# Optimization experiments

Hardware: AMD Instinct MI355X
Metric: run time of the kernel (lower is better)

## Reference

```python
import jax, jax.numpy as jnp
import numpy as np

DIM = 1024
NUM_HEADS = 16
HEAD_DIM = DIM // NUM_HEADS
ROPE_BASE = 10000.0


def _rope_tables(seq_len, head_dim, dtype):
    # inv_freq over even indices, then freqs duplicated (cat(freqs, freqs))
    inv_freq = 1.0 / (ROPE_BASE ** (jnp.arange(0, head_dim, 2, dtype=jnp.float32) / head_dim))
    t = jnp.arange(seq_len, dtype=jnp.float32)
    freqs = jnp.einsum('i,j->ij', t, inv_freq)          # [N, head_dim/2]
    emb = jnp.concatenate([freqs, freqs], axis=-1)      # [N, head_dim]
    return jnp.cos(emb).astype(dtype), jnp.sin(emb).astype(dtype)


def _rotate_half(x):
    x1, x2 = jnp.split(x, 2, axis=-1)
    return jnp.concatenate([-x2, x1], axis=-1)


def setup_inputs() -> dict:
    key = jax.random.key(0)
    k1, k2, k3 = jax.random.split(key, 3)
    B, N = 2, 2048
    x = jax.random.normal(k1, (B, N, DIM), dtype=jnp.float32)
    w_qkv = jax.random.normal(k2, (3 * DIM, DIM), dtype=jnp.float32) * (DIM ** -0.5)
    w_out = jax.random.normal(k3, (DIM, DIM), dtype=jnp.float32) * (DIM ** -0.5)
    return {"x": x, "w_qkv": w_qkv, "w_out": w_out}


def reference(x, w_qkv, w_out):
    B, N, C = x.shape
    scale = HEAD_DIM ** -0.5
    qkv = x @ w_qkv.T                                   # [B, N, 3*C]
    qkv = qkv.reshape(B, N, 3, NUM_HEADS, HEAD_DIM)
    qkv = jnp.transpose(qkv, (2, 0, 3, 1, 4))           # [3, B, H, N, hd]
    q, k, v = qkv[0], qkv[1], qkv[2]

    cos, sin = _rope_tables(N, HEAD_DIM, x.dtype)       # [N, hd] each
    q = q * cos + _rotate_half(q) * sin
    k = k * cos + _rotate_half(k) * sin

    attn = jnp.einsum('bhqd,bhkd->bhqk', q, k) * scale  # [B, H, N, N]
    attn = jax.nn.softmax(attn, axis=-1)
    out = jnp.einsum('bhqk,bhkd->bhqd', attn, v)        # [B, H, N, hd]
    out = jnp.transpose(out, (0, 2, 1, 3)).reshape(B, N, C)
    return out @ w_out.T
```

## Files before the change

### kernel.cpp

```cpp
#include <hip/hip_runtime.h>
#include <stdint.h>


#define BATCH 2
#define SEQ   2048
#define DIM_C 1024
#define NHEAD 16
#define HD    64
#define MTOT  (BATCH * SEQ)
#define NQKV  (3 * DIM_C)
#define QSCALE 0.1803368801111204f

typedef _Float16 h8 __attribute__((ext_vector_type(8)));
typedef _Float16 h4v __attribute__((ext_vector_type(4)));
typedef float    f4 __attribute__((ext_vector_type(4)));
typedef unsigned int u4v __attribute__((ext_vector_type(4)));

#if __has_builtin(__builtin_amdgcn_exp2f)
#define EXP2(x) __builtin_amdgcn_exp2f(x)
#else
#define EXP2(x) exp2f(x)
#endif

__device__ __forceinline__ f4 mfma16(h8 a, h8 b, f4 c) {
  return __builtin_amdgcn_mfma_f32_16x16x32_f16(a, b, c, 0, 0, 0);
}

__device__ __forceinline__ unsigned pk2(float a, float b) {
  auto t = __builtin_amdgcn_cvt_pkrtz(a, b);
  unsigned u;
  __builtin_memcpy(&u, &t, 4);
  return u;
}

__device__ __forceinline__ void swap32(unsigned& a, unsigned& b) {
#if __has_builtin(__builtin_amdgcn_permlane32_swap)
  typedef unsigned u2_ __attribute__((ext_vector_type(2)));
  u2_ r = __builtin_amdgcn_permlane32_swap(a, b, false, false);
  a = r[0]; b = r[1];
#else
  const bool hi = (threadIdx.x & 32) != 0;
  unsigned sa = __shfl_xor(a, 32), sb = __shfl_xor(b, 32);
  unsigned na = hi ? sb : a, nb = hi ? b : sa;
  a = na; b = nb;
#endif
}
__device__ __forceinline__ void swap16(unsigned& a, unsigned& b) {
#if __has_builtin(__builtin_amdgcn_permlane16_swap)
  typedef unsigned u2_ __attribute__((ext_vector_type(2)));
  u2_ r = __builtin_amdgcn_permlane16_swap(a, b, false, false);
  a = r[0]; b = r[1];
#else
  const bool hi = (threadIdx.x & 16) != 0;
  unsigned sa = __shfl_xor(a, 16), sb = __shfl_xor(b, 16);
  unsigned na = hi ? sb : a, nb = hi ? b : sa;
  a = na; b = nb;
#endif
}

__device__ __forceinline__ void gload16(const _Float16* g, _Float16* l) {
  __builtin_amdgcn_global_load_lds(
      (const __attribute__((address_space(1))) void*)g,
      (__attribute__((address_space(3))) void*)l, 16, 0, 0);
}

#define N4X  1048576
#define N4WQ 786432
#define N4WO 262144
#define CVT_TOT (N4X + N4WQ + N4WO)
__global__ void prep_kernel(const float* __restrict__ x,
                            const float* __restrict__ wq,
                            const float* __restrict__ wo,
                            _Float16* __restrict__ xh,
                            _Float16* __restrict__ wqh,
                            _Float16* __restrict__ woh,
                            float* __restrict__ cosT, float* __restrict__ sinT) {
  int idx = blockIdx.x * blockDim.x + threadIdx.x;
  if (idx < CVT_TOT) {
    const float* s; _Float16* d; int i;
    if (idx < N4X) { s = x; d = xh; i = idx; }
    else if (idx < N4X + N4WQ) { s = wq; d = wqh; i = idx - N4X; }
    else { s = wo; d = woh; i = idx - (N4X + N4WQ); }
    float4 v = reinterpret_cast<const float4*>(s)[i];
    h4v o = {(_Float16)v.x, (_Float16)v.y, (_Float16)v.z, (_Float16)v.w};
    reinterpret_cast<h4v*>(d)[i] = o;
  } else {
    int t = idx - CVT_TOT;
    int n = t >> 5, j = t & 31;
    float inv = powf(10000.0f, -(float)(2 * j) / 64.0f);
    float a = (float)n * inv;
    cosT[t] = cosf(a);
    sinT[t] = sinf(a);
  }
}

__global__ __launch_bounds__(256) void gemm_qkv(const _Float16* __restrict__ A,
                                                const _Float16* __restrict__ Bm,
                                                const float* __restrict__ cosT,
                                                const float* __restrict__ sinT,
                                                _Float16* __restrict__ qh,
                                                _Float16* __restrict__ kh,
                                                _Float16* __restrict__ vh) {
  const int K = DIM_C;
  __shared__ _Float16 Ah[2][128 * 32];
  __shared__ _Float16 Bh[2][128 * 32];
  const int tid = threadIdx.x;
  const int wave = tid >> 6, lane = tid & 63;
  const int lr = lane & 15, lg = lane >> 4;
  const int p = blockIdx.x;
  const int wg = (p & 7) * 96 + (p >> 3);
  const int bx = wg >> 5, by = wg & 31;
  const int m0 = by * 128, n0 = bx * 128;
  const int wr = (wave >> 1) * 64, wc = (wave & 1) * 64;

  const f4 zf = {0.f, 0.f, 0.f, 0.f};
  f4 acc[4][4];
#pragma unroll
  for (int i = 0; i < 4; ++i)
#pragma unroll
    for (int j = 0; j < 4; ++j) acc[i][j] = zf;

  const _Float16* Ab = A + (size_t)m0 * K;
  const _Float16* Bb = Bm + (size_t)n0 * K;

  auto stage = [&](int ks, int bi) {
#pragma unroll
    for (int it = 0; it < 2; ++it) {
      int c = tid + it * 256;
      int row = c >> 2, part = c & 3;
      gload16(Ab + (size_t)row * K + ks * 32 + part * 8, &Ah[bi][c * 8]);
      gload16(Bb + (size_t)row * K + ks * 32 + part * 8, &Bh[bi][c * 8]);
    }
  };

  stage(0, 0);
  const int ksteps = K >> 5;
  for (int ks = 0; ks < ksteps; ++ks) {
    __syncthreads();
    int cur = ks & 1;
    if (ks + 1 < ksteps) stage(ks + 1, cur ^ 1);

    h8 af[4], bf[4];
#pragma unroll
    for (int i = 0; i < 4; ++i) af[i] = *(const h8*)&Ah[cur][(wr + i * 16 + lr) * 32 + lg * 8];
#pragma unroll
    for (int j = 0; j < 4; ++j) bf[j] = *(const h8*)&Bh[cur][(wc + j * 16 + lr) * 32 + lg * 8];
#pragma unroll
    for (int i = 0; i < 4; ++i)
#pragma unroll
      for (int j = 0; j < 4; ++j) acc[i][j] = mfma16(af[i], bf[j], acc[i][j]);
  }

  const int nc = n0 + wc;
  const int s = nc >> 10;
  const int hcol = (nc >> 6) & 15;
  _Float16* dst = (s == 0) ? qh : (s == 1) ? kh : vh;
  const float scl = (s == 0) ? QSCALE : 1.0f;
#pragma unroll
  for (int i = 0; i < 4; ++i)
#pragma unroll
    for (int r = 0; r < 4; ++r) {
      int row = m0 + wr + i * 16 + lg * 4 + r;
      int n = row & (SEQ - 1);
      _Float16* drow = dst + ((size_t)(((row >> 11) * NHEAD + hcol) * SEQ + n)) * HD;
      if (s == 2) {
        drow[lr]      = (_Float16)acc[i][0][r];
        drow[lr + 16] = (_Float16)acc[i][1][r];
        drow[lr + 32] = (_Float16)acc[i][2][r];
        drow[lr + 48] = (_Float16)acc[i][3][r];
      } else {
        float c0 = cosT[n * 32 + lr],      sn0 = sinT[n * 32 + lr];
        float c1 = cosT[n * 32 + 16 + lr], sn1 = sinT[n * 32 + 16 + lr];
        float a10 = acc[i][0][r], a20 = acc[i][2][r];
        float a11 = acc[i][1][r], a21 = acc[i][3][r];
        drow[lr]      = (_Float16)((a10 * c0 - a20 * sn0) * scl);
        drow[lr + 32] = (_Float16)((a20 * c0 + a10 * sn0) * scl);
        drow[lr + 16] = (_Float16)((a11 * c1 - a21 * sn1) * scl);
        drow[lr + 48] = (_Float16)((a21 * c1 + a11 * sn1) * scl);
      }
    }
}

__global__ __launch_bounds__(256) void gemm_out(const _Float16* __restrict__ A,
                                                const _Float16* __restrict__ Bm,
                                                float* __restrict__ Cv) {
  const int K = DIM_C, N = DIM_C;
  __shared__ _Float16 Ah[2][128 * 32];
  __shared__ _Float16 Bh[2][64 * 32];
  const int tid = threadIdx.x;
  const int wave = tid >> 6, lane = tid & 63;
  const int lr = lane & 15, lg = lane >> 4;
  const int p = blockIdx.x;
  const int wg = (p & 7) * 64 + (p >> 3);
  const int bx = wg >> 5, by = wg & 31;
  const int m0 = by * 128, n0 = bx * 64;
  const int wr = (wave >> 1) * 64, wc = (wave & 1) * 32;

  const f4 zf = {0.f, 0.f, 0.f, 0.f};
  f4 acc[4][2];
#pragma unroll
  for (int i = 0; i < 4; ++i)
#pragma unroll
    for (int j = 0; j < 2; ++j) acc[i][j] = zf;

  const _Float16* Ab = A + (size_t)m0 * K;
  const _Float16* Bb = Bm + (size_t)n0 * K;

  auto stage = [&](int ks, int bi) {
#pragma unroll
    for (int it = 0; it < 2; ++it) {
      int c = tid + it * 256;
      int row = c >> 2, part = c & 3;
      gload16(Ab + (size_t)row * K + ks * 32 + part * 8, &Ah[bi][c * 8]);
    }
    int c = tid;
    gload16(Bb + (size_t)(c >> 2) * K + ks * 32 + (c & 3) * 8, &Bh[bi][c * 8]);
  };

  stage(0, 0);
  const int ksteps = K >> 5;
  for (int ks = 0; ks < ksteps; ++ks) {
    __syncthreads();
    int cur = ks & 1;
    if (ks + 1 < ksteps) stage(ks + 1, cur ^ 1);

    h8 af[4], bf[2];
#pragma unroll
    for (int i = 0; i < 4; ++i) af[i] = *(const h8*)&Ah[cur][(wr + i * 16 + lr) * 32 + lg * 8];
#pragma unroll
    for (int j = 0; j < 2; ++j) bf[j] = *(const h8*)&Bh[cur][(wc + j * 16 + lr) * 32 + lg * 8];
#pragma unroll
    for (int i = 0; i < 4; ++i)
#pragma unroll
      for (int j = 0; j < 2; ++j) acc[i][j] = mfma16(af[i], bf[j], acc[i][j]);
  }

#pragma unroll
  for (int i = 0; i < 4; ++i)
#pragma unroll
    for (int j = 0; j < 2; ++j)
#pragma unroll
      for (int r = 0; r < 4; ++r) {
        size_t row = (size_t)(m0 + wr + i * 16 + lg * 4 + r);
        int col = n0 + wc + j * 16 + lr;
        Cv[row * N + col] = acc[i][j][r];
      }
}

__global__ void vtrans_kernel(const _Float16* __restrict__ v, _Float16* __restrict__ vt) {
  int blk = blockIdx.x;
  int bh = blk >> 6, nt = blk & 63;
  int d = threadIdx.x & 63, w = threadIdx.x >> 6;
  int n0 = nt * 32 + w * 8;
  const _Float16* src = v + (size_t)bh * SEQ * HD;
  _Float16* dst = vt + ((size_t)bh * HD + d) * SEQ;
  h8 o;
#pragma unroll
  for (int j = 0; j < 8; ++j) o[j] = src[(size_t)(n0 + j) * HD + d];
  *(h8*)(dst + n0) = o;
}

__global__ __launch_bounds__(256, 2) void attn_kernel(const _Float16* __restrict__ qh,
                                                      const _Float16* __restrict__ kh,
                                                      const _Float16* __restrict__ vt,
                                                      _Float16* __restrict__ aoh) {
  __shared__ _Float16 Kt[2][128 * 64];
  __shared__ _Float16 Vt[2][64 * 128];

  const int tid = threadIdx.x, wave = tid >> 6, lane = tid & 63;
  const int lr = lane & 15, lg = lane >> 4;
  const int p = blockIdx.x;
  const int wg = (p & 7) * 64 + (p >> 3);
  const int bh = wg >> 4;
  const int qt = wg & 15;
  const int b = bh >> 4, h = bh & 15;

  const _Float16* Qb = qh + (size_t)bh * SEQ * HD;
  const _Float16* Kb = kh + (size_t)bh * SEQ * HD;
  const _Float16* Vb = vt + (size_t)bh * HD * SEQ;
  const int q0 = qt * 128 + wave * 32;

  int kOf[2], vOf[2][2];
#pragma unroll
  for (int cc = 0; cc < 2; ++cc) kOf[cc] = ((cc * 4 + lg) ^ (lr & 7)) * 8;
#pragma unroll
  for (int sub = 0; sub < 2; ++sub)
#pragma unroll
    for (int cc = 0; cc < 2; ++cc) vOf[sub][cc] = ((sub * 8 + cc * 4 + lg) ^ lr) * 8;

  h8 aq[2][2];
#pragma unroll
  for (int r2 = 0; r2 < 2; ++r2)
#pragma unroll
    for (int c = 0; c < 2; ++c)
      aq[r2][c] = *(const h8*)(Qb + (size_t)(q0 + r2 * 16 + lr) * HD + c * 32 + lg * 8);

  const h8 onesv = {(_Float16)1.f, (_Float16)1.f, (_Float16)1.f, (_Float16)1.f,
                    (_Float16)1.f, (_Float16)1.f, (_Float16)1.f, (_Float16)1.f};
  const f4 zf = {0.f, 0.f, 0.f, 0.f};
  f4 lacc[2] = {zf, zf};
  f4 acc[2][4];
#pragma unroll
  for (int r2 = 0; r2 < 2; ++r2)
#pragma unroll
    for (int dt = 0; dt < 4; ++dt) acc[r2][dt] = zf;

  auto stage = [&](int kt, int bi) {
    const _Float16* Ks = Kb + (size_t)kt * 128 * HD;
    const _Float16* Vs = Vb + kt * 128;
#pragma unroll
    for (int it = 0; it < 4; ++it) {
      int c = tid + it * 256;
      int krow = c >> 3, kpart = c & 7;
      int ksp = kpart ^ (krow & 7);
      gload16(Ks + (size_t)krow * HD + ksp * 8, &Kt[bi][c * 8]);
      int vrow = c >> 4, vpart = c & 15;
      int vsp = vpart ^ (vrow & 15);
      gload16(Vs + (size_t)vrow * SEQ + vsp * 8, &Vt[bi][c * 8]);
    }
  };

  stage(0, 0);
  for (int t = 0; t < SEQ / 128; ++t) {
    __syncthreads();
    const int cur = t & 1;
    if (t + 1 < SEQ / 128) stage(t + 1, cur ^ 1);

    const _Float16* Kbuf = &Kt[cur][0];
    const _Float16* Vbuf = &Vt[cur][0];
#pragma unroll
    for (int sub = 0; sub < 2; ++sub) {
      h8 bk[4][2], vb[4][2];
      const _Float16* Krow = Kbuf + (sub * 64 + lr) * 64;
#pragma unroll
      for (int ct = 0; ct < 4; ++ct)
#pragma unroll
        for (int cc = 0; cc < 2; ++cc)
          bk[ct][cc] = *(const h8*)(Krow + ct * 16 * 64 + kOf[cc]);
      const _Float16* Vrow = Vbuf + lr * 128;
#pragma unroll
      for (int dt = 0; dt < 4; ++dt)
#pragma unroll
        for (int cc = 0; cc < 2; ++cc)
          vb[dt][cc] = *(const h8*)(Vrow + dt * 16 * 128 + vOf[sub][cc]);

#pragma unroll
      for (int r2 = 0; r2 < 2; ++r2) {
        f4 St[4];
        __builtin_amdgcn_s_setprio(1);
#pragma unroll
        for (int ct = 0; ct < 4; ++ct) {
          f4 z = mfma16(bk[ct][0], aq[r2][0], zf);
          St[ct] = mfma16(bk[ct][1], aq[r2][1], z);
        }
        __builtin_amdgcn_s_setprio(0);

        unsigned w[4][2];
#pragma unroll
        for (int ct = 0; ct < 4; ++ct) {
          w[ct][0] = pk2(EXP2(St[ct][0]), EXP2(St[ct][1]));
          w[ct][1] = pk2(EXP2(St[ct][2]), EXP2(St[ct][3]));
        }
        swap32(w[0][0], w[1][0]); swap32(w[0][1], w[1][1]);
        swap32(w[2][0], w[3][0]); swap32(w[2][1], w[3][1]);
        swap16(w[0][0], w[1][0]); swap16(w[0][1], w[1][1]);
        swap16(w[2][0], w[3][0]); swap16(w[2][1], w[3][1]);
        u4v pw0 = {w[0][0], w[0][1], w[1][0], w[1][1]};
        u4v pw1 = {w[2][0], w[2][1], w[3][0], w[3][1]};
        h8 pa0, pa1;
        __builtin_memcpy(&pa0, &pw0, 16);
        __builtin_memcpy(&pa1, &pw1, 16);

        __builtin_amdgcn_s_setprio(1);
        lacc[r2] = mfma16(onesv, pa0, lacc[r2]);
        lacc[r2] = mfma16(onesv, pa1, lacc[r2]);
#pragma unroll
        for (int dt = 0; dt < 4; ++dt) {
          acc[r2][dt] = mfma16(vb[dt][0], pa0, acc[r2][dt]);
          acc[r2][dt] = mfma16(vb[dt][1], pa1, acc[r2][dt]);
        }
        __builtin_amdgcn_s_setprio(0);
      }
    }
  }

#pragma unroll
  for (int r2 = 0; r2 < 2; ++r2) {
    float inv = 1.0f / lacc[r2][0];
    int q = q0 + r2 * 16 + lr;
#pragma unroll
    for (int dt = 0; dt < 4; ++dt) {
      h4v o = {(_Float16)(acc[r2][dt][0] * inv), (_Float16)(acc[r2][dt][1] * inv),
               (_Float16)(acc[r2][dt][2] * inv), (_Float16)(acc[r2][dt][3] * inv)};
      *(h4v*)&aoh[((size_t)(b * SEQ + q)) * DIM_C + h * HD + dt * 16 + lg * 4] = o;
    }
  }
}

extern "C" void kernel_launch(void* const* d_in, const int* in_sizes, int n_in,
                              void* d_out, int out_size, void* d_ws, size_t ws_size,
                              hipStream_t stream) {
  const float* x     = (const float*)d_in[0];
  const float* w_qkv = (const float*)d_in[1];
  const float* w_out = (const float*)d_in[2];
  float* out = (float*)d_out;

  char* w = (char*)d_ws;
  _Float16* xh    = (_Float16*)(w + 0);
  _Float16* wqkvh = (_Float16*)(w + 8388608);
  _Float16* wouth = (_Float16*)(w + 14680064);
  _Float16* qhp   = (_Float16*)(w + 16777216);
  _Float16* khp   = (_Float16*)(w + 25165824);
  _Float16* vhp   = (_Float16*)(w + 33554432);
  _Float16* vtp   = (_Float16*)(w + 41943040);
  _Float16* aohp  = (_Float16*)(w + 50331648);
  float*    cosT  = (float*)(w + 58720256);
  float*    sinT  = (float*)(w + 58982400);

  prep_kernel<<<(CVT_TOT + SEQ * 32) / 256, 256, 0, stream>>>(
      x, w_qkv, w_out, xh, wqkvh, wouth, cosT, sinT);

  gemm_qkv<<<768, 256, 0, stream>>>(xh, wqkvh, cosT, sinT, qhp, khp, vhp);

  vtrans_kernel<<<32 * 64, 256, 0, stream>>>(vhp, vtp);

  attn_kernel<<<32 * 16, 256, 0, stream>>>(qhp, khp, vtp, aohp);

  gemm_out<<<512, 256, 0, stream>>>(aohp, wouth, out);
}
```

Before: 132.0 us.

## Swizzle GEMM LDS tiles and load attention K/V directly from global

Both GEMMs now store their A and B tiles in LDS as 64-wide rows, pairing two source rows with an XOR swizzle, to cut bank conflicts on the MFMA fragment reads. The attention kernel drops its LDS double-buffered K/V staging and the barriers that went with it. Each wave instead loads its K and V fragments straight from global memory (relying on L1/L2), with the loop unrolled by two. This removes LDS traffic and synchronisation in attention. The cost is redundant global loads across the four waves and exposed load latency.

```diff
diff --git a/kernel.cpp b/kernel.cpp
--- a/kernel.cpp
+++ b/kernel.cpp
@@ -102,8 +102,8 @@
                                                 _Float16* __restrict__ kh,
                                                 _Float16* __restrict__ vh) {
   const int K = DIM_C;
-  __shared__ _Float16 Ah[2][128 * 32];
-  __shared__ _Float16 Bh[2][128 * 32];
+  __shared__ _Float16 Ah[2][64 * 64];
+  __shared__ _Float16 Bh[2][64 * 64];
   const int tid = threadIdx.x;
   const int wave = tid >> 6, lane = tid & 63;
   const int lr = lane & 15, lg = lane >> 4;
@@ -127,11 +127,16 @@
 #pragma unroll
     for (int it = 0; it < 2; ++it) {
       int c = tid + it * 256;
-      int row = c >> 2, part = c & 3;
-      gload16(Ab + (size_t)row * K + ks * 32 + part * 8, &Ah[bi][c * 8]);
-      gload16(Bb + (size_t)row * K + ks * 32 + part * 8, &Bh[bi][c * 8]);
+      int lrow = c >> 3;
+      int sch = (c & 7) ^ (lrow & 7);
+      int mrow = lrow * 2 + (sch >> 2), part = sch & 3;
+      gload16(Ab + (size_t)mrow * K + ks * 32 + part * 8, &Ah[bi][c * 8]);
+      gload16(Bb + (size_t)mrow * K + ks * 32 + part * 8, &Bh[bi][c * 8]);
     }
   };
+
+  const int rch = (((lr & 1) * 4 + lg) ^ (lr >> 1)) * 8;
+  const int lrb = lr >> 1;
 
   stage(0, 0);
   const int ksteps = K >> 5;
@@ -142,9 +147,11 @@
 
     h8 af[4], bf[4];
 #pragma unroll
-    for (int i = 0; i < 4; ++i) af[i] = *(const h8*)&Ah[cur][(wr + i * 16 + lr) * 32 + lg * 8];
-#pragma unroll
-    for (int j = 0; j < 4; ++j) bf[j] = *(const h8*)&Bh[cur][(wc + j * 16 + lr) * 32 + lg * 8];
+    for (int i = 0; i < 4; ++i)
+      af[i] = *(const h8*)&Ah[cur][(wr / 2 + i * 8 + lrb) * 64 + rch];
+#pragma unroll
+    for (int j = 0; j < 4; ++j)
+      bf[j] = *(const h8*)&Bh[cur][(wc / 2 + j * 8 + lrb) * 64 + rch];
 #pragma unroll
     for (int i = 0; i < 4; ++i)
 #pragma unroll
@@ -185,8 +192,8 @@
                                                 const _Float16* __restrict__ Bm,
                                                 float* __restrict__ Cv) {
   const int K = DIM_C, N = DIM_C;
-  __shared__ _Float16 Ah[2][128 * 32];
-  __shared__ _Float16 Bh[2][64 * 32];
+  __shared__ _Float16 Ah[2][64 * 64];
+  __shared__ _Float16 Bh[2][32 * 64];
   const int tid = threadIdx.x;
   const int wave = tid >> 6, lane = tid & 63;
   const int lr = lane & 15, lg = lane >> 4;
@@ -210,12 +217,20 @@
 #pragma unroll
     for (int it = 0; it < 2; ++it) {
       int c = tid + it * 256;
-      int row = c >> 2, part = c & 3;
-      gload16(Ab + (size_t)row * K + ks * 32 + part * 8, &Ah[bi][c * 8]);
+      int lrow = c >> 3;
+      int sch = (c & 7) ^ (lrow & 7);
+      int mrow = lrow * 2 + (sch >> 2), part = sch & 3;
+      gload16(Ab + (size_t)mrow * K + ks * 32 + part * 8, &Ah[bi][c * 8]);
     }
     int c = tid;
-    gload16(Bb + (size_t)(c >> 2) * K + ks * 32 + (c & 3) * 8, &Bh[bi][c * 8]);
+    int lrow = c >> 3;
+    int sch = (c & 7) ^ (lrow & 7);
+    int mrow = lrow * 2 + (sch >> 2), part = sch & 3;
+    gload16(Bb + (size_t)mrow * K + ks * 32 + part * 8, &Bh[bi][c * 8]);
   };
+
+  const int rch = (((lr & 1) * 4 + lg) ^ (lr >> 1)) * 8;
+  const int lrb = lr >> 1;
 
   stage(0, 0);
   const int ksteps = K >> 5;
@@ -226,9 +241,11 @@
 
     h8 af[4], bf[2];
 #pragma unroll
-    for (int i = 0; i < 4; ++i) af[i] = *(const h8*)&Ah[cur][(wr + i * 16 + lr) * 32 + lg * 8];
-#pragma unroll
-    for (int j = 0; j < 2; ++j) bf[j] = *(const h8*)&Bh[cur][(wc + j * 16 + lr) * 32 + lg * 8];
+    for (int i = 0; i < 4; ++i)
+      af[i] = *(const h8*)&Ah[cur][(wr / 2 + i * 8 + lrb) * 64 + rch];
+#pragma unroll
+    for (int j = 0; j < 2; ++j)
+      bf[j] = *(const h8*)&Bh[cur][(wc / 2 + j * 8 + lrb) * 64 + rch];
 #pragma unroll
     for (int i = 0; i < 4; ++i)
 #pragma unroll
@@ -264,9 +281,6 @@
                                                       const _Float16* __restrict__ kh,
                                                       const _Float16* __restrict__ vt,
                                                       _Float16* __restrict__ aoh) {
-  __shared__ _Float16 Kt[2][128 * 64];
-  __shared__ _Float16 Vt[2][64 * 128];
-
   const int tid = threadIdx.x, wave = tid >> 6, lane = tid & 63;
   const int lr = lane & 15, lg = lane >> 4;
   const int p = blockIdx.x;
@@ -280,14 +294,6 @@
   const _Float16* Vb = vt + (size_t)bh * HD * SEQ;
   const int q0 = qt * 128 + wave * 32;
 
-  int kOf[2], vOf[2][2];
-#pragma unroll
-  for (int cc = 0; cc < 2; ++cc) kOf[cc] = ((cc * 4 + lg) ^ (lr & 7)) * 8;
-#pragma unroll
-  for (int sub = 0; sub < 2; ++sub)
-#pragma unroll
-    for (int cc = 0; cc < 2; ++cc) vOf[sub][cc] = ((sub * 8 + cc * 4 + lg) ^ lr) * 8;
-
   h8 aq[2][2];
 #pragma unroll
   for (int r2 = 0; r2 < 2; ++r2)
@@ -305,82 +311,61 @@
 #pragma unroll
     for (int dt = 0; dt < 4; ++dt) acc[r2][dt] = zf;
 
-  auto stage = [&](int kt, int bi) {
-    const _Float16* Ks = Kb + (size_t)kt * 128 * HD;
-    const _Float16* Vs = Vb + kt * 128;
-#pragma unroll
-    for (int it = 0; it < 4; ++it) {
-      int c = tid + it * 256;
-      int krow = c >> 3, kpart = c & 7;
-      int ksp = kpart ^ (krow & 7);
-      gload16(Ks + (size_t)krow * HD + ksp * 8, &Kt[bi][c * 8]);
-      int vrow = c >> 4, vpart = c & 15;
-      int vsp = vpart ^ (vrow & 15);
-      gload16(Vs + (size_t)vrow * SEQ + vsp * 8, &Vt[bi][c * 8]);
-    }
-  };
-
-  stage(0, 0);
-  for (int t = 0; t < SEQ / 128; ++t) {
-    __syncthreads();
-    const int cur = t & 1;
-    if (t + 1 < SEQ / 128) stage(t + 1, cur ^ 1);
-
-    const _Float16* Kbuf = &Kt[cur][0];
-    const _Float16* Vbuf = &Vt[cur][0];
-#pragma unroll
-    for (int sub = 0; sub < 2; ++sub) {
-      h8 bk[4][2], vb[4][2];
-      const _Float16* Krow = Kbuf + (sub * 64 + lr) * 64;
-#pragma unroll
-      for (int ct = 0; ct < 4; ++ct)
-#pragma unroll
-        for (int cc = 0; cc < 2; ++cc)
-          bk[ct][cc] = *(const h8*)(Krow + ct * 16 * 64 + kOf[cc]);
-      const _Float16* Vrow = Vbuf + lr * 128;
-#pragma unroll
-      for (int dt = 0; dt < 4; ++dt)
-#pragma unroll
-        for (int cc = 0; cc < 2; ++cc)
-          vb[dt][cc] = *(const h8*)(Vrow + dt * 16 * 128 + vOf[sub][cc]);
-
-#pragma unroll
-      for (int r2 = 0; r2 < 2; ++r2) {
-        f4 St[4];
-        __builtin_amdgcn_s_setprio(1);
-#pragma unroll
-        for (int ct = 0; ct < 4; ++ct) {
-          f4 z = mfma16(bk[ct][0], aq[r2][0], zf);
-          St[ct] = mfma16(bk[ct][1], aq[r2][1], z);
-        }
-        __builtin_amdgcn_s_setprio(0);
-
-        unsigned w[4][2];
-#pragma unroll
-        for (int ct = 0; ct < 4; ++ct) {
-          w[ct][0] = pk2(EXP2(St[ct][0]), EXP2(St[ct][1]));
-          w[ct][1] = pk2(EXP2(St[ct][2]), EXP2(St[ct][3]));
-        }
-        swap32(w[0][0], w[1][0]); swap32(w[0][1], w[1][1]);
-        swap32(w[2][0], w[3][0]); swap32(w[2][1], w[3][1]);
-        swap16(w[0][0], w[1][0]); swap16(w[0][1], w[1][1]);
-        swap16(w[2][0], w[3][0]); swap16(w[2][1], w[3][1]);
-        u4v pw0 = {w[0][0], w[0][1], w[1][0], w[1][1]};
-        u4v pw1 = {w[2][0], w[2][1], w[3][0], w[3][1]};
-        h8 pa0, pa1;
-        __builtin_memcpy(&pa0, &pw0, 16);
-        __builtin_memcpy(&pa1, &pw1, 16);
-
-        __builtin_amdgcn_s_setprio(1);
-        lacc[r2] = mfma16(onesv, pa0, lacc[r2]);
-        lacc[r2] = mfma16(onesv, pa1, lacc[r2]);
-#pragma unroll
-        for (int dt = 0; dt < 4; ++dt) {
-          acc[r2][dt] = mfma16(vb[dt][0], pa0, acc[r2][dt]);
-          acc[r2][dt] = mfma16(vb[dt][1], pa1, acc[r2][dt]);
-        }
-        __builtin_amdgcn_s_setprio(0);
+  const _Float16* Kp = Kb + (size_t)lr * HD + lg * 8;
+  const _Float16* Vp = Vb + (size_t)lr * SEQ + lg * 8;
+
+#pragma unroll 2
+  for (int s = 0; s < SEQ / 64; ++s) {
+    h8 kf[4][2], vf[4][2];
+    const _Float16* Ks = Kp + (size_t)s * 64 * HD;
+#pragma unroll
+    for (int ct = 0; ct < 4; ++ct)
+#pragma unroll
+      for (int cc = 0; cc < 2; ++cc)
+        kf[ct][cc] = *(const h8*)(Ks + ct * 16 * HD + cc * 32);
+    const _Float16* Vs = Vp + s * 64;
+#pragma unroll
+    for (int dt = 0; dt < 4; ++dt)
+#pragma unroll
+      for (int cc = 0; cc < 2; ++cc)
+        vf[dt][cc] = *(const h8*)(Vs + (size_t)dt * 16 * SEQ + cc * 32);
+
+#pragma unroll
+    for (int r2 = 0; r2 < 2; ++r2) {
+      f4 St[4];
+      __builtin_amdgcn_s_setprio(1);
+#pragma unroll
+      for (int ct = 0; ct < 4; ++ct) {
+        f4 z = mfma16(kf[ct][0], aq[r2][0], zf);
+        St[ct] = mfma16(kf[ct][1], aq[r2][1], z);
       }
+      __builtin_amdgcn_s_setprio(0);
+
+      unsigned w[4][2];
+#pragma unroll
+      for (int ct = 0; ct < 4; ++ct) {
+        w[ct][0] = pk2(EXP2(St[ct][0]), EXP2(St[ct][1]));
+        w[ct][1] = pk2(EXP2(St[ct][2]), EXP2(St[ct][3]));
+      }
+      swap32(w[0][0], w[1][0]); swap32(w[0][1], w[1][1]);
+      swap32(w[2][0], w[3][0]); swap32(w[2][1], w[3][1]);
+      swap16(w[0][0], w[1][0]); swap16(w[0][1], w[1][1]);
+      swap16(w[2][0], w[3][0]); swap16(w[2][1], w[3][1]);
+      u4v pw0 = {w[0][0], w[0][1], w[1][0], w[1][1]};
+      u4v pw1 = {w[2][0], w[2][1], w[3][0], w[3][1]};
+      h8 pa0, pa1;
+      __builtin_memcpy(&pa0, &pw0, 16);
+      __builtin_memcpy(&pa1, &pw1, 16);
+
+      __builtin_amdgcn_s_setprio(1);
+      lacc[r2] = mfma16(onesv, pa0, lacc[r2]);
+      lacc[r2] = mfma16(onesv, pa1, lacc[r2]);
+#pragma unroll
+      for (int dt = 0; dt < 4; ++dt) {
+        acc[r2][dt] = mfma16(vf[dt][0], pa0, acc[r2][dt]);
+        acc[r2][dt] = mfma16(vf[dt][1], pa1, acc[r2][dt]);
+      }
+      __builtin_amdgcn_s_setprio(0);
     }
   }
 
```

After: 202.6 us. 1.54x slower.

## Swizzle GEMM shared-memory tiles and vectorize QKV epilogue with permuted head layout

Applied to the files above, without the earlier changes.

Both GEMM kernels now stage A/B tiles into shared memory as 64-half rows that pack two source rows, with an XOR swizzle on 16-byte chunks. The MFMA fragment reads use matching swizzled addresses, which is meant to cut LDS bank conflicts. The QKV epilogue writes four halves per lane as one vector store instead of four scalar stores. To allow that, it permutes the head-dim order in q/k/v. q·k is unaffected because both use the same permutation, and the V transpose kernel undoes the permutation, so the address logic now spans three kernels.

```diff
diff --git a/kernel.cpp b/kernel.cpp
--- a/kernel.cpp
+++ b/kernel.cpp
@@ -102,8 +102,8 @@
                                                 _Float16* __restrict__ kh,
                                                 _Float16* __restrict__ vh) {
   const int K = DIM_C;
-  __shared__ _Float16 Ah[2][128 * 32];
-  __shared__ _Float16 Bh[2][128 * 32];
+  __shared__ _Float16 Ah[2][64 * 64];
+  __shared__ _Float16 Bh[2][64 * 64];
   const int tid = threadIdx.x;
   const int wave = tid >> 6, lane = tid & 63;
   const int lr = lane & 15, lg = lane >> 4;
@@ -127,11 +127,16 @@
 #pragma unroll
     for (int it = 0; it < 2; ++it) {
       int c = tid + it * 256;
-      int row = c >> 2, part = c & 3;
-      gload16(Ab + (size_t)row * K + ks * 32 + part * 8, &Ah[bi][c * 8]);
-      gload16(Bb + (size_t)row * K + ks * 32 + part * 8, &Bh[bi][c * 8]);
+      int lrow = c >> 3;
+      int sch = (c & 7) ^ (lrow & 7);
+      int mrow = lrow * 2 + (sch >> 2), part = sch & 3;
+      gload16(Ab + (size_t)mrow * K + ks * 32 + part * 8, &Ah[bi][c * 8]);
+      gload16(Bb + (size_t)mrow * K + ks * 32 + part * 8, &Bh[bi][c * 8]);
     }
   };
+
+  const int rch = (((lr & 1) * 4 + lg) ^ (lr >> 1)) * 8;
+  const int lrb = lr >> 1;
 
   stage(0, 0);
   const int ksteps = K >> 5;
@@ -142,9 +147,11 @@
 
     h8 af[4], bf[4];
 #pragma unroll
-    for (int i = 0; i < 4; ++i) af[i] = *(const h8*)&Ah[cur][(wr + i * 16 + lr) * 32 + lg * 8];
-#pragma unroll
-    for (int j = 0; j < 4; ++j) bf[j] = *(const h8*)&Bh[cur][(wc + j * 16 + lr) * 32 + lg * 8];
+    for (int i = 0; i < 4; ++i)
+      af[i] = *(const h8*)&Ah[cur][(wr / 2 + i * 8 + lrb) * 64 + rch];
+#pragma unroll
+    for (int j = 0; j < 4; ++j)
+      bf[j] = *(const h8*)&Bh[cur][(wc / 2 + j * 8 + lrb) * 64 + rch];
 #pragma unroll
     for (int i = 0; i < 4; ++i)
 #pragma unroll
@@ -163,21 +170,21 @@
       int row = m0 + wr + i * 16 + lg * 4 + r;
       int n = row & (SEQ - 1);
       _Float16* drow = dst + ((size_t)(((row >> 11) * NHEAD + hcol) * SEQ + n)) * HD;
+      h4v o;
       if (s == 2) {
-        drow[lr]      = (_Float16)acc[i][0][r];
-        drow[lr + 16] = (_Float16)acc[i][1][r];
-        drow[lr + 32] = (_Float16)acc[i][2][r];
-        drow[lr + 48] = (_Float16)acc[i][3][r];
+        o = {(_Float16)acc[i][0][r], (_Float16)acc[i][1][r],
+             (_Float16)acc[i][2][r], (_Float16)acc[i][3][r]};
       } else {
         float c0 = cosT[n * 32 + lr],      sn0 = sinT[n * 32 + lr];
         float c1 = cosT[n * 32 + 16 + lr], sn1 = sinT[n * 32 + 16 + lr];
         float a10 = acc[i][0][r], a20 = acc[i][2][r];
         float a11 = acc[i][1][r], a21 = acc[i][3][r];
-        drow[lr]      = (_Float16)((a10 * c0 - a20 * sn0) * scl);
-        drow[lr + 32] = (_Float16)((a20 * c0 + a10 * sn0) * scl);
-        drow[lr + 16] = (_Float16)((a11 * c1 - a21 * sn1) * scl);
-        drow[lr + 48] = (_Float16)((a21 * c1 + a11 * sn1) * scl);
+        o = {(_Float16)((a10 * c0 - a20 * sn0) * scl),
+             (_Float16)((a11 * c1 - a21 * sn1) * scl),
+             (_Float16)((a20 * c0 + a10 * sn0) * scl),
+             (_Float16)((a21 * c1 + a11 * sn1) * scl)};
       }
+      *(h4v*)&drow[lr * 4] = o;
     }
 }
 
@@ -185,8 +192,8 @@
                                                 const _Float16* __restrict__ Bm,
                                                 float* __restrict__ Cv) {
   const int K = DIM_C, N = DIM_C;
-  __shared__ _Float16 Ah[2][128 * 32];
-  __shared__ _Float16 Bh[2][64 * 32];
+  __shared__ _Float16 Ah[2][64 * 64];
+  __shared__ _Float16 Bh[2][32 * 64];
   const int tid = threadIdx.x;
   const int wave = tid >> 6, lane = tid & 63;
   const int lr = lane & 15, lg = lane >> 4;
@@ -210,12 +217,20 @@
 #pragma unroll
     for (int it = 0; it < 2; ++it) {
       int c = tid + it * 256;
-      int row = c >> 2, part = c & 3;
-      gload16(Ab + (size_t)row * K + ks * 32 + part * 8, &Ah[bi][c * 8]);
+      int lrow = c >> 3;
+      int sch = (c & 7) ^ (lrow & 7);
+      int mrow = lrow * 2 + (sch >> 2), part = sch & 3;
+      gload16(Ab + (size_t)mrow * K + ks * 32 + part * 8, &Ah[bi][c * 8]);
     }
     int c = tid;
-    gload16(Bb + (size_t)(c >> 2) * K + ks * 32 + (c & 3) * 8, &Bh[bi][c * 8]);
+    int lrow = c >> 3;
+    int sch = (c & 7) ^ (lrow & 7);
+    int mrow = lrow * 2 + (sch >> 2), part = sch & 3;
+    gload16(Bb + (size_t)mrow * K + ks * 32 + part * 8, &Bh[bi][c * 8]);
   };
+
+  const int rch = (((lr & 1) * 4 + lg) ^ (lr >> 1)) * 8;
+  const int lrb = lr >> 1;
 
   stage(0, 0);
   const int ksteps = K >> 5;
@@ -226,9 +241,11 @@
 
     h8 af[4], bf[2];
 #pragma unroll
-    for (int i = 0; i < 4; ++i) af[i] = *(const h8*)&Ah[cur][(wr + i * 16 + lr) * 32 + lg * 8];
-#pragma unroll
-    for (int j = 0; j < 2; ++j) bf[j] = *(const h8*)&Bh[cur][(wc + j * 16 + lr) * 32 + lg * 8];
+    for (int i = 0; i < 4; ++i)
+      af[i] = *(const h8*)&Ah[cur][(wr / 2 + i * 8 + lrb) * 64 + rch];
+#pragma unroll
+    for (int j = 0; j < 2; ++j)
+      bf[j] = *(const h8*)&Bh[cur][(wc / 2 + j * 8 + lrb) * 64 + rch];
 #pragma unroll
     for (int i = 0; i < 4; ++i)
 #pragma unroll
@@ -251,12 +268,13 @@
   int blk = blockIdx.x;
   int bh = blk >> 6, nt = blk & 63;
   int d = threadIdx.x & 63, w = threadIdx.x >> 6;
+  int pp = (d & 15) * 4 + (d >> 4);
   int n0 = nt * 32 + w * 8;
   const _Float16* src = v + (size_t)bh * SEQ * HD;
   _Float16* dst = vt + ((size_t)bh * HD + d) * SEQ;
   h8 o;
 #pragma unroll
-  for (int j = 0; j < 8; ++j) o[j] = src[(size_t)(n0 + j) * HD + d];
+  for (int j = 0; j < 8; ++j) o[j] = src[(size_t)(n0 + j) * HD + pp];
   *(h8*)(dst + n0) = o;
 }
 
```

Measured after the change: 129.3 us. 2.0% less time.
